# Optimization experiments

Measured on AMD Instinct MI355X. Metric: run time of the kernel, lower is better.

## Reference

```python
import jax, jax.numpy as jnp
import numpy as np

BATCH_SIZE = 4096
TEMPERATURE = 0.5
DIAG_NEG = -50000.0
EPS = 1e-8  # torch CosineSimilarity eps


def setup_inputs() -> dict:
    key = jax.random.key(0)
    k1, k2 = jax.random.split(key)
    z_i = jax.random.normal(k1, (BATCH_SIZE, 128), dtype=jnp.float32)
    z_j = jax.random.normal(k2, (BATCH_SIZE, 128), dtype=jnp.float32)
    return {"z_i": z_i, "z_j": z_j}


def reference(z_i, z_j):
    n = z_i.shape[0]
    z = jnp.concatenate([z_i, z_j], axis=0)  # [2N, D]
    # cosine similarity: normalize once, then one GEMM (same math as
    # CosineSimilarity(dim=2) on the broadcasted pair, with eps clamp on norms)
    norms = jnp.maximum(jnp.linalg.norm(z, axis=-1, keepdims=True), EPS)
    zn = z / norms
    sim = (zn @ zn.T) / TEMPERATURE  # [2N, 2N]
    # mask self-similarity on the diagonal
    idx = jnp.arange(2 * n)
    sim = sim.at[idx, idx].set(DIAG_NEG)
    # labels: positive pair is the other view
    labels = jnp.concatenate([idx[n:], idx[:n]])  # [2N]
    # mean softmax cross-entropy
    logp = jax.nn.log_softmax(sim, axis=-1)
    loss = -jnp.mean(logp[idx, labels])
    return loss
```

## Files before the change

kernel.cpp:

```cpp
#include <hip/hip_runtime.h>

#define N2 8192
#define NHALF 4096
#define DDIM 128
#define NCHUNK 16
#define CPC 512
#define NT 8
#define LN2F 0.69314718055994530942f
#define SCALEF 1.6986436f

typedef __attribute__((ext_vector_type(8))) short bf8_t;
typedef __attribute__((ext_vector_type(4))) float f4_t;

__device__ __forceinline__ float fexp2(float x) { return __builtin_amdgcn_exp2f(x); }
__device__ __forceinline__ float flog2(float x) { return __builtin_amdgcn_logf(x); }

__device__ __forceinline__ unsigned short f2bf(float f) {
  unsigned int x = __float_as_uint(f);
  x += 0x7fffu + ((x >> 16) & 1u);
  return (unsigned short)(x >> 16);
}
__device__ __forceinline__ float bf2f(unsigned short h) {
  return __uint_as_float(((unsigned int)h) << 16);
}

__global__ __launch_bounds__(256) void knorm(const float* __restrict__ zi,
                                             const float* __restrict__ zj,
                                             unsigned short* __restrict__ u,
                                             float* __restrict__ dhat) {
  const int lane = threadIdx.x & 63;
  const int row = blockIdx.x * 4 + (threadIdx.x >> 6);
  const float* src = (row < NHALF) ? (zi + (size_t)row * DDIM)
                                   : (zj + (size_t)(row - NHALF) * DDIM);
  float2 x = *(const float2*)(src + lane * 2);
  float ss = x.x * x.x + x.y * x.y;
#pragma unroll
  for (int m = 32; m; m >>= 1) ss += __shfl_xor(ss, m);
  float scale = SCALEF / fmaxf(sqrtf(ss), 1e-8f);
  unsigned short b0 = f2bf(x.x * scale);
  unsigned short b1 = f2bf(x.y * scale);
  *(unsigned int*)(u + (size_t)row * DDIM + lane * 2) =
      (unsigned int)b0 | ((unsigned int)b1 << 16);
  float f0 = bf2f(b0), f1 = bf2f(b1);
  float dd = f0 * f0 + f1 * f1;
#pragma unroll
  for (int m = 32; m; m >>= 1) dd += __shfl_xor(dd, m);
  if (lane == 0) dhat[row] = dd;
}

__global__ __launch_bounds__(512) void ksim(const unsigned short* __restrict__ u,
                                            float* __restrict__ Lp) {
  __shared__ short Bls[24576];
  const int tid = threadIdx.x;
  const int lane = tid & 63;
  const int w = tid >> 6;
  const int rb = blockIdx.x >> 4;
  const int chunk = blockIdx.x & 15;
  const int lr = lane & 15, lq = lane >> 4;
  const int rowbase = rb * 256 + w * 32;
  const int colbase = chunk * CPC;

  bf8_t a[2][4];
#pragma unroll
  for (int s = 0; s < 2; s++)
#pragma unroll
    for (int kc = 0; kc < 4; kc++)
      a[s][kc] = *(const bf8_t*)(u + (size_t)(rowbase + s * 16 + lr) * DDIM +
                                 kc * 32 + lq * 8);
#pragma unroll
  for (int s = 0; s < 2; s++)
#pragma unroll
    for (int kc = 0; kc < 4; kc++)
      asm volatile("" : "+v"(a[s][kc]));

  f4_t L0 = {0.f, 0.f, 0.f, 0.f}, L1 = {0.f, 0.f, 0.f, 0.f};

  auto STAGE = [&](int t) {
#pragma unroll
    for (int i = 0; i < 2; i++) {
      const int j = w * 2 + i;
      const int col_local = j * 4 + lq;
      const int sdu = lr ^ (4 * (j & 1) + lq);
      const unsigned short* src =
          u + (size_t)(colbase + t * 64 + col_local) * DDIM + sdu * 8;
      short* dst = &Bls[(t % 3) * 8192 + j * 512];
      __builtin_amdgcn_global_load_lds(
          (const __attribute__((address_space(1))) unsigned int*)src,
          (__attribute__((address_space(3))) unsigned int*)dst, 16, 0, 0);
    }
  };

  auto COMP = [&](int t) {
    const short* P = &Bls[(t % 3) * 8192];
#pragma unroll
    for (int g = 0; g < 4; g++) {
      bf8_t bv[4];
#pragma unroll
      for (int kc = 0; kc < 4; kc++)
        bv[kc] = *(const bf8_t*)&P[((g * 16 + lr) * 16 +
                                    ((kc * 4 + lq) ^ (lr & 7))) * 8];
      f4_t acc0 = {0.f, 0.f, 0.f, 0.f}, acc1 = {0.f, 0.f, 0.f, 0.f};
#pragma unroll
      for (int kc = 0; kc < 4; kc++) {
        acc0 = __builtin_amdgcn_mfma_f32_16x16x32_bf16(a[0][kc], bv[kc], acc0, 0, 0, 0);
        acc1 = __builtin_amdgcn_mfma_f32_16x16x32_bf16(a[1][kc], bv[kc], acc1, 0, 0, 0);
      }
#pragma unroll
      for (int r = 0; r < 4; r++) {
        L0[r] += fexp2(acc0[r]);
        L1[r] += fexp2(acc1[r]);
      }
    }
  };

  STAGE(0);
  STAGE(1);
#pragma unroll 1
  for (int t = 0; t < NT; ++t) {
    if (t < NT - 1) {
      asm volatile("s_waitcnt vmcnt(2)" ::: "memory");
    } else {
      asm volatile("s_waitcnt vmcnt(0)" ::: "memory");
    }
    __builtin_amdgcn_sched_barrier(0);
    __builtin_amdgcn_s_barrier();
    __builtin_amdgcn_sched_barrier(0);
    COMP(t);
    if (t + 2 < NT) STAGE(t + 2);
  }

#pragma unroll
  for (int r = 0; r < 4; r++) {
    float v0 = L0[r], v1 = L1[r];
    v0 += __shfl_xor(v0, 1); v0 += __shfl_xor(v0, 2);
    v0 += __shfl_xor(v0, 4); v0 += __shfl_xor(v0, 8);
    v1 += __shfl_xor(v1, 1); v1 += __shfl_xor(v1, 2);
    v1 += __shfl_xor(v1, 4); v1 += __shfl_xor(v1, 8);
    if (lr == 0) {
      const int rrow = rowbase + lq * 4 + r;
      Lp[(size_t)chunk * N2 + rrow] = v0;
      Lp[(size_t)chunk * N2 + rrow + 16] = v1;
    }
  }
}

__global__ __launch_bounds__(256) void krow(const unsigned short* __restrict__ u,
                                            const float* __restrict__ dhat,
                                            const float* __restrict__ Lp,
                                            float* __restrict__ bsum) {
  const int i = blockIdx.x * 256 + threadIdx.x;
  float L = 0.f;
#pragma unroll
  for (int c = 0; c < NCHUNK; c++) L += Lp[(size_t)c * N2 + i];
  L -= fexp2(dhat[i]);

  const int j = (i + NHALF) & (N2 - 1);
  const unsigned int* ui = (const unsigned int*)(u + (size_t)i * DDIM);
  const unsigned int* uj = (const unsigned int*)(u + (size_t)j * DDIM);
  float dot = 0.f;
#pragma unroll
  for (int k = 0; k < DDIM / 2; k++) {
    unsigned int av = ui[k], bv = uj[k];
    dot += __uint_as_float(av << 16) * __uint_as_float(bv << 16) +
           __uint_as_float(av & 0xffff0000u) * __uint_as_float(bv & 0xffff0000u);
  }
  float loss = LN2F * (flog2(L) - dot);

#pragma unroll
  for (int m = 32; m; m >>= 1) loss += __shfl_xor(loss, m);
  __shared__ float sred[4];
  if ((threadIdx.x & 63) == 0) sred[threadIdx.x >> 6] = loss;
  __syncthreads();
  if (threadIdx.x == 0) bsum[blockIdx.x] = sred[0] + sred[1] + sred[2] + sred[3];
}

__global__ void kfinal(const float* __restrict__ bsum, float* __restrict__ out) {
  float v = (threadIdx.x < N2 / 256) ? bsum[threadIdx.x] : 0.f;
#pragma unroll
  for (int m = 32; m; m >>= 1) v += __shfl_xor(v, m);
  if (threadIdx.x == 0) out[0] = v * (1.0f / N2);
}

extern "C" void kernel_launch(void* const* d_in, const int* in_sizes, int n_in,
                              void* d_out, int out_size, void* d_ws, size_t ws_size,
                              hipStream_t stream) {
  const float* zi = (const float*)d_in[0];
  const float* zj = (const float*)d_in[1];
  char* ws = (char*)d_ws;
  unsigned short* u = (unsigned short*)ws;
  float* dhat = (float*)(ws + (size_t)N2 * DDIM * 2);
  float* Lp = (float*)(ws + (size_t)N2 * DDIM * 2 + (size_t)N2 * 4);
  float* bsum = (float*)(ws + (size_t)N2 * DDIM * 2 + (size_t)N2 * 4 +
                         (size_t)NCHUNK * N2 * 4);
  float* out = (float*)d_out;

  hipLaunchKernelGGL(knorm, dim3(N2 / 4), dim3(256), 0, stream, zi, zj, u, dhat);
  hipLaunchKernelGGL(ksim, dim3((N2 / 256) * NCHUNK), dim3(512), 0, stream, u, Lp);
  hipLaunchKernelGGL(krow, dim3(N2 / 256), dim3(256), 0, stream, u, dhat, Lp, bsum);
  hipLaunchKernelGGL(kfinal, dim3(1), dim3(64), 0, stream, bsum, out);
}
```

Baseline: 37.54 us.

## Widen sim blocks to 1024 threads and parallelize row loss per wavefront

The similarity kernel now uses 1024-thread blocks covering 512 rows, so each staged B tile in LDS is reused by twice as many wavefronts and each wave issues one async global-to-LDS load per stage. The partial row sums are stored row-major so the row kernel can read them contiguously. The row kernel now gives each row a full wavefront, computing the positive-pair dot product and the chunk-sum reduction with shuffles instead of one serial 128-element loop per thread. The final reduction sums 2048 block partials. The larger blocks halve the grid to 256 blocks and may lower occupancy.

```diff
diff --git a/kernel.cpp b/kernel.cpp
--- a/kernel.cpp
+++ b/kernel.cpp
@@ -6,6 +6,7 @@
 #define NCHUNK 16
 #define CPC 512
 #define NT 8
+#define RPB 512
 #define LN2F 0.69314718055994530942f
 #define SCALEF 1.6986436f
 
@@ -48,8 +49,8 @@
   if (lane == 0) dhat[row] = dd;
 }
 
-__global__ __launch_bounds__(512) void ksim(const unsigned short* __restrict__ u,
-                                            float* __restrict__ Lp) {
+__global__ __launch_bounds__(1024) void ksim(const unsigned short* __restrict__ u,
+                                             float* __restrict__ Lp) {
   __shared__ short Bls[24576];
   const int tid = threadIdx.x;
   const int lane = tid & 63;
@@ -57,7 +58,7 @@
   const int rb = blockIdx.x >> 4;
   const int chunk = blockIdx.x & 15;
   const int lr = lane & 15, lq = lane >> 4;
-  const int rowbase = rb * 256 + w * 32;
+  const int rowbase = rb * RPB + w * 32;
   const int colbase = chunk * CPC;
 
   bf8_t a[2][4];
@@ -76,18 +77,14 @@
   f4_t L0 = {0.f, 0.f, 0.f, 0.f}, L1 = {0.f, 0.f, 0.f, 0.f};
 
   auto STAGE = [&](int t) {
-#pragma unroll
-    for (int i = 0; i < 2; i++) {
-      const int j = w * 2 + i;
-      const int col_local = j * 4 + lq;
-      const int sdu = lr ^ (4 * (j & 1) + lq);
-      const unsigned short* src =
-          u + (size_t)(colbase + t * 64 + col_local) * DDIM + sdu * 8;
-      short* dst = &Bls[(t % 3) * 8192 + j * 512];
-      __builtin_amdgcn_global_load_lds(
-          (const __attribute__((address_space(1))) unsigned int*)src,
-          (__attribute__((address_space(3))) unsigned int*)dst, 16, 0, 0);
-    }
+    const int col_local = w * 4 + lq;
+    const int sdu = lr ^ (4 * (w & 1) + lq);
+    const unsigned short* src =
+        u + (size_t)(colbase + t * 64 + col_local) * DDIM + sdu * 8;
+    short* dst = &Bls[(t % 3) * 8192 + w * 512];
+    __builtin_amdgcn_global_load_lds(
+        (const __attribute__((address_space(1))) unsigned int*)src,
+        (__attribute__((address_space(3))) unsigned int*)dst, 16, 0, 0);
   };
 
   auto COMP = [&](int t) {
@@ -118,7 +115,7 @@
 #pragma unroll 1
   for (int t = 0; t < NT; ++t) {
     if (t < NT - 1) {
-      asm volatile("s_waitcnt vmcnt(2)" ::: "memory");
+      asm volatile("s_waitcnt vmcnt(1)" ::: "memory");
     } else {
       asm volatile("s_waitcnt vmcnt(0)" ::: "memory");
     }
@@ -138,8 +135,8 @@
     v1 += __shfl_xor(v1, 4); v1 += __shfl_xor(v1, 8);
     if (lr == 0) {
       const int rrow = rowbase + lq * 4 + r;
-      Lp[(size_t)chunk * N2 + rrow] = v0;
-      Lp[(size_t)chunk * N2 + rrow + 16] = v1;
+      Lp[(size_t)rrow * NCHUNK + chunk] = v0;
+      Lp[(size_t)(rrow + 16) * NCHUNK + chunk] = v1;
     }
   }
 }
@@ -148,34 +145,35 @@
                                             const float* __restrict__ dhat,
                                             const float* __restrict__ Lp,
                                             float* __restrict__ bsum) {
-  const int i = blockIdx.x * 256 + threadIdx.x;
-  float L = 0.f;
+  const int lane = threadIdx.x & 63;
+  const int w = threadIdx.x >> 6;
+  const int i = blockIdx.x * 4 + w;
+  const int j = (i + NHALF) & (N2 - 1);
+
+  const unsigned int av = ((const unsigned int*)(u + (size_t)i * DDIM))[lane];
+  const unsigned int bv = ((const unsigned int*)(u + (size_t)j * DDIM))[lane];
+  float dot = __uint_as_float(av << 16) * __uint_as_float(bv << 16) +
+              __uint_as_float(av & 0xffff0000u) * __uint_as_float(bv & 0xffff0000u);
+  float ls = (lane < NCHUNK) ? Lp[(size_t)i * NCHUNK + lane] : 0.f;
 #pragma unroll
-  for (int c = 0; c < NCHUNK; c++) L += Lp[(size_t)c * N2 + i];
-  L -= fexp2(dhat[i]);
-
-  const int j = (i + NHALF) & (N2 - 1);
-  const unsigned int* ui = (const unsigned int*)(u + (size_t)i * DDIM);
-  const unsigned int* uj = (const unsigned int*)(u + (size_t)j * DDIM);
-  float dot = 0.f;
-#pragma unroll
-  for (int k = 0; k < DDIM / 2; k++) {
-    unsigned int av = ui[k], bv = uj[k];
-    dot += __uint_as_float(av << 16) * __uint_as_float(bv << 16) +
-           __uint_as_float(av & 0xffff0000u) * __uint_as_float(bv & 0xffff0000u);
+  for (int m = 32; m; m >>= 1) {
+    dot += __shfl_xor(dot, m);
+    ls += __shfl_xor(ls, m);
   }
-  float loss = LN2F * (flog2(L) - dot);
-
-#pragma unroll
-  for (int m = 32; m; m >>= 1) loss += __shfl_xor(loss, m);
   __shared__ float sred[4];
-  if ((threadIdx.x & 63) == 0) sred[threadIdx.x >> 6] = loss;
+  if (lane == 0) {
+    const float L = ls - fexp2(dhat[i]);
+    sred[w] = LN2F * (flog2(L) - dot);
+  }
   __syncthreads();
-  if (threadIdx.x == 0) bsum[blockIdx.x] = sred[0] + sred[1] + sred[2] + sred[3];
+  if (threadIdx.x == 0)
+    bsum[blockIdx.x] = sred[0] + sred[1] + sred[2] + sred[3];
 }
 
 __global__ void kfinal(const float* __restrict__ bsum, float* __restrict__ out) {
-  float v = (threadIdx.x < N2 / 256) ? bsum[threadIdx.x] : 0.f;
+  float v = 0.f;
+#pragma unroll
+  for (int jj = 0; jj < 32; jj++) v += bsum[threadIdx.x + 64 * jj];
 #pragma unroll
   for (int m = 32; m; m >>= 1) v += __shfl_xor(v, m);
   if (threadIdx.x == 0) out[0] = v * (1.0f / N2);
@@ -195,7 +193,7 @@
   float* out = (float*)d_out;
 
   hipLaunchKernelGGL(knorm, dim3(N2 / 4), dim3(256), 0, stream, zi, zj, u, dhat);
-  hipLaunchKernelGGL(ksim, dim3((N2 / 256) * NCHUNK), dim3(512), 0, stream, u, Lp);
-  hipLaunchKernelGGL(krow, dim3(N2 / 256), dim3(256), 0, stream, u, dhat, Lp, bsum);
+  hipLaunchKernelGGL(ksim, dim3((N2 / RPB) * NCHUNK), dim3(1024), 0, stream, u, Lp);
+  hipLaunchKernelGGL(krow, dim3(N2 / 4), dim3(256), 0, stream, u, dhat, Lp, bsum);
   hipLaunchKernelGGL(kfinal, dim3(1), dim3(64), 0, stream, bsum, out);
 }
```

New measurement: 36.31 us. 3.3% less time.
